# Kernel tuning notes

Measured on AMD Instinct MI355X. Metric: run time of the kernel, lower is better.

## Reference

```python
import jax, jax.numpy as jnp
import numpy as np

N, H, W, C, G, K = 8, 64, 64, 128, 8, 3
GC = C // G          # group channels = 16
P = K * K            # 9 sampling points
PAD = DIL = STRIDE = 1
OS = 1.0             # offset_scale
EPS = 1e-6
H_IN, W_IN = H + 2 * PAD, W + 2 * PAD


def _grid_sample_nhwc(img, grid):
    # img: (B, Hi, Wi, Cc) ; grid: (B, L, Pp, 2) in [-1,1]
    # bilinear, padding_mode='zeros', align_corners=False (matches F.grid_sample)
    B, Hi, Wi, Cc = img.shape
    gx = (grid[..., 0] + 1.0) * (Wi * 0.5) - 0.5
    gy = (grid[..., 1] + 1.0) * (Hi * 0.5) - 0.5
    x0 = jnp.floor(gx)
    y0 = jnp.floor(gy)
    wx1 = gx - x0
    wy1 = gy - y0
    b = jnp.arange(B).reshape(B, 1, 1)

    def tap(xi, yi, wgt):
        valid = (xi >= 0) & (xi <= Wi - 1) & (yi >= 0) & (yi <= Hi - 1)
        xc = jnp.clip(xi, 0, Wi - 1).astype(jnp.int32)
        yc = jnp.clip(yi, 0, Hi - 1).astype(jnp.int32)
        return img[b, yc, xc] * (wgt * valid)[..., None]

    return (tap(x0, y0, (1 - wx1) * (1 - wy1))
            + tap(x0 + 1, y0, wx1 * (1 - wy1))
            + tap(x0, y0 + 1, (1 - wx1) * wy1)
            + tap(x0 + 1, y0 + 1, wx1 * wy1))


def _forward(x, w_in, b_in, dw_w, dw_b, ln_g, ln_b, w_off, b_off, w_msk, b_msk, w_out, b_out):
    n = x.shape[0]
    x_proj = x @ w_in + b_in                                  # input_proj (n,H,W,C)
    # dw_conv: depthwise 3x3 -> LayerNorm(channels_last) -> GELU
    x1 = jax.lax.conv_general_dilated(
        x, dw_w, (1, 1), [((K - 1) // 2,) * 2] * 2,
        dimension_numbers=('NHWC', 'HWIO', 'NHWC'), feature_group_count=C) + dw_b
    mu = jnp.mean(x1, -1, keepdims=True)
    var = jnp.mean((x1 - mu) ** 2, -1, keepdims=True)
    x1 = (x1 - mu) * jax.lax.rsqrt(var + EPS) * ln_g + ln_b
    x1 = jax.nn.gelu(x1, approximate=False)
    offset = x1 @ w_off + b_off                               # (n,H,W,G*P*2)
    mask = jax.nn.softmax((x1 @ w_msk + b_msk).reshape(n, H, W, G, P), axis=-1)
    # reference points on the padded input (pixel-center, normalized)
    ry = (DIL * (K - 1) // 2 + 0.5 + jnp.arange(H, dtype=jnp.float32) * STRIDE) / H_IN
    rx = (DIL * (K - 1) // 2 + 0.5 + jnp.arange(W, dtype=jnp.float32) * STRIDE) / W_IN
    ref = jnp.stack([jnp.broadcast_to(rx[None, :], (H, W)),
                     jnp.broadcast_to(ry[:, None], (H, W))], -1)      # (H,W,2) = (x,y)
    # dilation kernel grid, x-major flatten (matches torch meshgrid indexing='ij')
    ks = jnp.arange(K, dtype=jnp.float32) * DIL - DIL * (K - 1) // 2
    gxk, gyk = jnp.meshgrid(ks, ks, indexing='ij')
    pts = jnp.stack([gxk / W_IN, gyk / H_IN], -1).reshape(P, 2)
    pts = jnp.tile(pts, (G, 1))                                       # (G*P,2), group-major
    loc = (ref[:, :, None, :] + pts[None, None, :, :] * OS).reshape(1, H, W, G * P * 2)
    snorm = jnp.tile(jnp.array([W_IN, H_IN], jnp.float32), G * P)     # [w,h,w,h,...]
    loc = loc + offset * OS / snorm
    grids = (2.0 * loc - 1.0).reshape(n, H * W, G, P, 2)
    grids = grids.transpose(0, 2, 1, 3, 4).reshape(n * G, H * W, P, 2)
    x_pad = jnp.pad(x_proj, ((0, 0), (PAD, PAD), (PAD, PAD), (0, 0)))
    img = x_pad.reshape(n, H_IN, W_IN, G, GC).transpose(0, 3, 1, 2, 4).reshape(n * G, H_IN, W_IN, GC)
    sampled = _grid_sample_nhwc(img, grids)                            # (n*G, HW, P, GC)
    m = mask.reshape(n, H * W, G, P).transpose(0, 2, 1, 3).reshape(n * G, H * W, P)
    out = (sampled * m[..., None]).sum(2)                              # (n*G, HW, GC)
    out = out.reshape(n, G, H * W, GC).transpose(0, 2, 1, 3).reshape(n, H, W, C)
    return out @ w_out + b_out                                         # output_proj


def setup_inputs():
    key = jax.random.key(0)
    k = jax.random.split(key, 8)
    s = 0.02
    f = jnp.float32
    return {
        'x': jax.random.normal(k[0], (N, H, W, C), f),
        'w_in': jax.random.normal(k[1], (C, C), f) * (1.0 / np.sqrt(C)),
        'b_in': jnp.zeros((C,), f),
        'dw_w': jax.random.normal(k[2], (K, K, 1, C), f) * s,
        'dw_b': jnp.zeros((C,), f),
        'ln_g': jnp.ones((C,), f),
        'ln_b': jnp.zeros((C,), f),
        'w_off': jax.random.normal(k[3], (C, G * P * 2), f) * s,
        'b_off': jax.random.normal(k[4], (G * P * 2,), f) * s,
        'w_msk': jax.random.normal(k[5], (C, G * P), f) * s,
        'b_msk': jnp.zeros((G * P,), f),
        'w_out': jax.random.normal(k[6], (C, C), f) * (1.0 / np.sqrt(C)),
        'b_out': jnp.zeros((C,), f),
    }


def reference(x, w_in, b_in, dw_w, dw_b, ln_g, ln_b, w_off, b_off, w_msk, b_msk, w_out, b_out):
    return _forward(x, w_in, b_in, dw_w, dw_b, ln_g, ln_b, w_off, b_off, w_msk, b_msk, w_out, b_out)
```

## Files before the change

kernel.cpp:

```cpp
#include <hip/hip_runtime.h>
#include <math.h>

#define NB 8
#define H 64
#define W 64
#define C 128
#define G 8
#define GC 16
#define P 9
#define NPIX (NB * H * W)
#define N_OFF 144
#define N_MSK 72
#define PXB 32
#define RECW 232
#define PK_IN_ELEMS   (8 * 4 * 64 * 8)
#define PK_COMB_ELEMS (14 * 4 * 64 * 8)
#define PK_OUT_ELEMS  (8 * 4 * 64 * 8)

using bf16x8 = __attribute__((ext_vector_type(8))) short;
using f32x4  = __attribute__((ext_vector_type(4))) float;
using u32x4  = __attribute__((ext_vector_type(4))) unsigned;

__device__ __forceinline__ short f2bf(float f) {
    union { float fv; unsigned u; } v; v.fv = f;
    unsigned r = v.u + 0x7fffu + ((v.u >> 16) & 1u);
    return (short)(r >> 16);
}

__global__ __launch_bounds__(256) void k_pack(
    const float* __restrict__ w_in, const float* __restrict__ w_off,
    const float* __restrict__ w_msk, const float* __restrict__ w_out,
    short* __restrict__ pk_in, short* __restrict__ pk_comb, short* __restrict__ pk_out)
{
    const int tid = blockIdx.x * 256 + threadIdx.x;
    int p, which;
    if (tid < PK_IN_ELEMS) { p = tid; which = 0; }
    else if (tid < PK_IN_ELEMS + PK_COMB_ELEMS) { p = tid - PK_IN_ELEMS; which = 1; }
    else if (tid < PK_IN_ELEMS + PK_COMB_ELEMS + PK_OUT_ELEMS) { p = tid - PK_IN_ELEMS - PK_COMB_ELEMS; which = 2; }
    else return;
    const int e = p & 7, lane = (p >> 3) & 63, kt = (p >> 9) & 3, nt = p >> 11;
    const int k = kt * 32 + (lane >> 4) * 8 + e;
    const int n = nt * 16 + (lane & 15);
    float v;
    if (which == 0) {
        v = w_in[k * C + n];
        pk_in[p] = f2bf(v);
    } else if (which == 1) {
        if (n < N_OFF) v = w_off[k * N_OFF + n];
        else if (n < N_OFF + N_MSK) v = w_msk[k * N_MSK + (n - N_OFF)];
        else v = 0.f;
        pk_comb[p] = f2bf(v);
    } else {
        v = w_out[k * C + n];
        pk_out[p] = f2bf(v);
    }
}

__global__ __launch_bounds__(256, 2) void k_front(
    const float* __restrict__ x, const short* __restrict__ pk_in,
    const float* __restrict__ b_in, unsigned short* __restrict__ xproj)
{
    const int t = threadIdx.x;
    const int n = blockIdx.x & 7;
    const int local = blockIdx.x >> 3;
    const int y = local >> 1;
    const int xb = (local & 1) * PXB;
    const int gpix0 = (n * H + y) * W + xb;

    const int w = t >> 6, l = t & 63;
    bf16x8 aA[2][4];
    #pragma unroll
    for (int mt = 0; mt < 2; ++mt) {
        const int m = mt * 16 + (l & 15);
        const float* rp = x + (size_t)(gpix0 + m) * C + (l >> 4) * 8;
        #pragma unroll
        for (int kt = 0; kt < 4; ++kt) {
            f32x4 v0 = *(const f32x4*)(rp + kt * 32);
            f32x4 v1 = *(const f32x4*)(rp + kt * 32 + 4);
            bf16x8 pk;
            #pragma unroll
            for (int e = 0; e < 4; ++e) { pk[e] = f2bf(v0[e]); pk[4 + e] = f2bf(v1[e]); }
            aA[mt][kt] = pk;
        }
    }
    #pragma unroll
    for (int i = 0; i < 2; ++i) {
        const int nt = w + i * 4;
        bf16x8 bf[4];
        const short* bp = pk_in + nt * 2048 + l * 8;
        #pragma unroll
        for (int kt = 0; kt < 4; ++kt) bf[kt] = *(const bf16x8*)(bp + kt * 512);
        const float bias = b_in[nt * 16 + (l & 15)];
        #pragma unroll
        for (int mt = 0; mt < 2; ++mt) {
            f32x4 acc = {0.f, 0.f, 0.f, 0.f};
            #pragma unroll
            for (int kt = 0; kt < 4; ++kt)
                acc = __builtin_amdgcn_mfma_f32_16x16x32_bf16(aA[mt][kt], bf[kt], acc, 0, 0, 0);
            const int prow = gpix0 + mt * 16 + (l >> 4) * 4;
            #pragma unroll
            for (int r = 0; r < 4; ++r)
                xproj[(size_t)(nt * NPIX + prow + r) * 16 + (l & 15)] =
                    (unsigned short)f2bf(acc[r] + bias);
        }
    }
}

__global__ __launch_bounds__(256, 2) void k_back(
    const float* __restrict__ x, const float* __restrict__ dw_w,
    const float* __restrict__ dw_b, const float* __restrict__ ln_g,
    const float* __restrict__ ln_b, const short* __restrict__ pk_comb,
    const float* __restrict__ b_off, const float* __restrict__ b_msk,
    const unsigned short* __restrict__ xproj, const short* __restrict__ pk_out,
    const float* __restrict__ b_out, float* __restrict__ out)
{
    __shared__ __align__(16) short buf0[PXB * C];
    __shared__ unsigned short recs[PXB * RECW];

    const int t = threadIdx.x;
    const int n = blockIdx.x & 7;
    const int local = blockIdx.x >> 3;
    const int y = local >> 1;
    const int xb = (local & 1) * PXB;
    const int gpix0 = (n * H + y) * W + xb;
    const int imgbase = n * (H * W);

    const int px = t >> 3;
    const int c8 = t & 7;
    const int cb = c8 * 4;
    const int sw = (px & 7) << 4;

    float a[16];
    #pragma unroll
    for (int q = 0; q < 4; ++q) {
        f32x4 v = *(const f32x4*)(dw_b + cb + q * 32);
        #pragma unroll
        for (int e = 0; e < 4; ++e) a[q * 4 + e] = v[e];
    }
    #pragma unroll
    for (int ky = 0; ky < 3; ++ky) {
        const int yy = y + ky - 1;
        if (yy < 0 || yy >= H) continue;
        #pragma unroll
        for (int kx = 0; kx < 3; ++kx) {
            const int xx = xb + px + kx - 1;
            if (xx < 0 || xx >= W) continue;
            const float* xp = x + ((size_t)(n * H + yy) * W + xx) * C;
            const float* wp = dw_w + (ky * 3 + kx) * C;
            #pragma unroll
            for (int q = 0; q < 4; ++q) {
                f32x4 xv = *(const f32x4*)(xp + cb + q * 32);
                f32x4 wv = *(const f32x4*)(wp + cb + q * 32);
                #pragma unroll
                for (int e = 0; e < 4; ++e)
                    a[q * 4 + e] = fmaf(xv[e], wv[e], a[q * 4 + e]);
            }
        }
    }
    float mu, rsg;
    {
        float s = 0.f, sq = 0.f;
        #pragma unroll
        for (int cc = 0; cc < 16; ++cc) { s += a[cc]; sq = fmaf(a[cc], a[cc], sq); }
        #pragma unroll
        for (int d = 1; d < 8; d <<= 1) {
            s += __shfl_xor(s, d);
            sq += __shfl_xor(sq, d);
        }
        mu = s * (1.0f / C);
        const float va = sq * (1.0f / C) - mu * mu;
        rsg = rsqrtf(va + 1e-6f);
    }
    #pragma unroll
    for (int q = 0; q < 4; ++q) {
        f32x4 gv = *(const f32x4*)(ln_g + cb + q * 32);
        f32x4 bv = *(const f32x4*)(ln_b + cb + q * 32);
        unsigned short h4[4];
        #pragma unroll
        for (int e = 0; e < 4; ++e) {
            float v = (a[q * 4 + e] - mu) * rsg * gv[e] + bv[e];
            h4[e] = (unsigned short)f2bf(v * 0.5f * (1.f + erff(v * 0.70710678118654752f)));
        }
        const unsigned lo = ((unsigned)h4[0]) | (((unsigned)h4[1]) << 16);
        const unsigned hi = ((unsigned)h4[2]) | (((unsigned)h4[3]) << 16);
        *(unsigned long long*)((char*)buf0 + px * 256 + ((cb * 2 + q * 64) ^ sw)) =
            ((unsigned long long)hi << 32) | lo;
    }
    __syncthreads();

    {
        const int w = t >> 6, l = t & 63;
        const int swA = (l & 7) << 4;
        bf16x8 aB[2][4];
        #pragma unroll
        for (int mt = 0; mt < 2; ++mt) {
            const int m = mt * 16 + (l & 15);
            #pragma unroll
            for (int kt = 0; kt < 4; ++kt)
                aB[mt][kt] = *(const bf16x8*)((char*)buf0 + m * 256 +
                                              ((kt * 64 + (l >> 4) * 16) ^ swA));
        }
        #pragma unroll
        for (int i = 0; i < 4; ++i) {
            const int nt = w + i * 4;
            if (nt < 14) {
                bf16x8 bf[4];
                const short* bp = pk_comb + nt * 2048 + l * 8;
                #pragma unroll
                for (int kt = 0; kt < 4; ++kt) bf[kt] = *(const bf16x8*)(bp + kt * 512);
                const int col = nt * 16 + (l & 15);
                int dcol = col;
                float bias = 0.f;
                bool valid = true;
                if (col < N_OFF) bias = b_off[col];
                else {
                    const int cm = col - N_OFF;
                    if (cm < N_MSK) {
                        const int g = (cm * 57) >> 9;
                        dcol = 144 + g * 10 + (cm - 9 * g);
                        bias = b_msk[cm];
                    } else valid = false;
                }
                #pragma unroll
                for (int mt = 0; mt < 2; ++mt) {
                    f32x4 acc = {0.f, 0.f, 0.f, 0.f};
                    #pragma unroll
                    for (int kt = 0; kt < 4; ++kt)
                        acc = __builtin_amdgcn_mfma_f32_16x16x32_bf16(aB[mt][kt], bf[kt], acc, 0, 0, 0);
                    if (valid) {
                        const int pr0 = mt * 16 + (l >> 4) * 4;
                        #pragma unroll
                        for (int r = 0; r < 4; ++r)
                            recs[(pr0 + r) * RECW + dcol] = (unsigned short)f2bf(acc[r] + bias);
                    }
                }
            }
        }
    }
    __syncthreads();

    {
        const int spx = t >> 3, g = t & 7;
        unsigned short* row = recs + spx * RECW + 144 + g * 10;
        float lg[P];
        #pragma unroll
        for (int p = 0; p < P; ++p) lg[p] = __uint_as_float(((unsigned)row[p]) << 16);
        float mx = lg[0];
        #pragma unroll
        for (int p2 = 1; p2 < P; ++p2) mx = fmaxf(mx, lg[p2]);
        float e[P], s = 0.f;
        #pragma unroll
        for (int p2 = 0; p2 < P; ++p2) { e[p2] = expf(lg[p2] - mx); s += e[p2]; }
        const float inv = 1.0f / s;
        #pragma unroll
        for (int p2 = 0; p2 < P; ++p2) row[p2] = (unsigned short)f2bf(e[p2] * inv);
    }
    __syncthreads();

    {
        const int spx = t & 31, g = t >> 5;
        const int xabs = xb + spx;
        const int swz = (spx & 7) << 4;
        const unsigned* rec32 = (const unsigned*)recs + spx * (RECW / 2);
        const unsigned short* prp = recs + spx * RECW + 144 + g * 10;

        float cf[25];
        #pragma unroll
        for (int i = 0; i < 25; ++i) cf[i] = 0.f;
        float amax = 0.f;
        #pragma unroll
        for (int p = 0; p < P; ++p) {
            const unsigned ovp = rec32[g * 9 + p];
            const float m = __uint_as_float(((unsigned)prp[p]) << 16);
            const float ox = __uint_as_float(ovp << 16);
            const float oy = __uint_as_float(ovp & 0xffff0000u);
            amax = fmaxf(amax, fmaxf(fabsf(ox), fabsf(oy)));
            const float fx = floorf(ox);
            const float fy = floorf(oy);
            const float wx = ox - fx, wy = oy - fy;
            const bool lox = fx < -0.5f;
            const bool loy = fy < -0.5f;
            const float wc0 = lox ? (1.f - wx) : 0.f;
            const float wc1 = lox ? wx : (1.f - wx);
            const float wc2 = lox ? 0.f : wx;
            const float wr0 = loy ? (1.f - wy) : 0.f;
            const float wr1 = loy ? wy : (1.f - wy);
            const float wr2 = loy ? 0.f : wy;
            const float mr0 = m * wr0, mr1 = m * wr1, mr2 = m * wr2;
            const int base = (p % 3) * 5 + (p / 3);
            cf[base + 0]  = fmaf(wc0, mr0, cf[base + 0]);
            cf[base + 1]  = fmaf(wc1, mr0, cf[base + 1]);
            cf[base + 2]  = fmaf(wc2, mr0, cf[base + 2]);
            cf[base + 5]  = fmaf(wc0, mr1, cf[base + 5]);
            cf[base + 6]  = fmaf(wc1, mr1, cf[base + 6]);
            cf[base + 7]  = fmaf(wc2, mr1, cf[base + 7]);
            cf[base + 10] = fmaf(wc0, mr2, cf[base + 10]);
            cf[base + 11] = fmaf(wc1, mr2, cf[base + 11]);
            cf[base + 12] = fmaf(wc2, mr2, cf[base + 12]);
        }
        #pragma unroll
        for (int j = 0; j < 5; ++j) {
            const int xc = xabs + j - 2;
            if (!((xc >= 0) & (xc < W))) {
                #pragma unroll
                for (int i = 0; i < 5; ++i) cf[i * 5 + j] = 0.f;
            }
        }
        #pragma unroll
        for (int i = 0; i < 5; ++i) {
            const int yc = y + i - 2;
            if (!((yc >= 0) & (yc < H))) {
                #pragma unroll
                for (int j = 0; j < 5; ++j) cf[i * 5 + j] = 0.f;
            }
        }
        const char* pb = (const char*)(xproj + (size_t)(g * NPIX + imgbase) * 16);
        int rowoff[5], coloff[5];
        #pragma unroll
        for (int i = 0; i < 5; ++i) {
            rowoff[i] = min(max(y + i - 2, 0), H - 1) * (W * 32);
            coloff[i] = min(max(xabs + i - 2, 0), W - 1) * 32;
        }

        float acc[16];
        #pragma unroll
        for (int q = 0; q < 16; ++q) acc[q] = 0.f;

        if (amax < 1.0f) {
            #pragma unroll
            for (int i = 0; i < 5; ++i) {
                #pragma unroll
                for (int j = 0; j < 5; ++j) {
                    const float c = cf[i * 5 + j];
                    const char* ap = pb + (rowoff[i] + coloff[j]);
                    u32x4 v0 = *(const u32x4*)ap;
                    u32x4 v1 = *(const u32x4*)(ap + 16);
                    #pragma unroll
                    for (int e = 0; e < 4; ++e) {
                        acc[2 * e]         = fmaf(c, __uint_as_float(v0[e] << 16), acc[2 * e]);
                        acc[2 * e + 1]     = fmaf(c, __uint_as_float(v0[e] & 0xffff0000u), acc[2 * e + 1]);
                        acc[8 + 2 * e]     = fmaf(c, __uint_as_float(v1[e] << 16), acc[8 + 2 * e]);
                        acc[8 + 2 * e + 1] = fmaf(c, __uint_as_float(v1[e] & 0xffff0000u), acc[8 + 2 * e + 1]);
                    }
                }
            }
        } else {
            for (int p = 0; p < P; ++p) {
                const unsigned ovp = rec32[g * 9 + p];
                const float m = __uint_as_float(((unsigned)prp[p]) << 16);
                const float ux = (float)(xabs + (p / 3) - 1) + __uint_as_float(ovp << 16);
                const float uy = (float)(y + (p % 3) - 1) + __uint_as_float(ovp & 0xffff0000u);
                const float fx = floorf(ux), fy = floorf(uy);
                const float wx = ux - fx, wy = uy - fy;
                const int x0 = (int)fx, y0 = (int)fy;
                float w4[4];
                w4[0] = m * (1.f - wx) * (1.f - wy);
                w4[1] = m * wx * (1.f - wy);
                w4[2] = m * (1.f - wx) * wy;
                w4[3] = m * wx * wy;
                if (!((x0 >= 0) & (x0 < W)))       { w4[0] = 0.f; w4[2] = 0.f; }
                if (!((x0 >= -1) & (x0 < W - 1)))  { w4[1] = 0.f; w4[3] = 0.f; }
                if (!((y0 >= 0) & (y0 < H)))       { w4[0] = 0.f; w4[1] = 0.f; }
                if (!((y0 >= -1) & (y0 < H - 1)))  { w4[2] = 0.f; w4[3] = 0.f; }
                const int xc[2] = { min(max(x0, 0), W - 1), min(max(x0 + 1, 0), W - 1) };
                const int yc[2] = { min(max(y0, 0), H - 1), min(max(y0 + 1, 0), H - 1) };
                for (int cn = 0; cn < 4; ++cn) {
                    const float wgt = w4[cn];
                    if (wgt == 0.f) continue;
                    const char* ap = pb + ((size_t)(yc[cn >> 1] * W + xc[cn & 1]) * 32);
                    u32x4 v0 = *(const u32x4*)ap;
                    u32x4 v1 = *(const u32x4*)(ap + 16);
                    #pragma unroll
                    for (int e = 0; e < 4; ++e) {
                        acc[2 * e]         = fmaf(wgt, __uint_as_float(v0[e] << 16), acc[2 * e]);
                        acc[2 * e + 1]     = fmaf(wgt, __uint_as_float(v0[e] & 0xffff0000u), acc[2 * e + 1]);
                        acc[8 + 2 * e]     = fmaf(wgt, __uint_as_float(v1[e] << 16), acc[8 + 2 * e]);
                        acc[8 + 2 * e + 1] = fmaf(wgt, __uint_as_float(v1[e] & 0xffff0000u), acc[8 + 2 * e + 1]);
                    }
                }
            }
        }
        __syncthreads();
        #pragma unroll
        for (int h = 0; h < 2; ++h) {
            bf16x8 pk;
            #pragma unroll
            for (int e = 0; e < 8; ++e) pk[e] = f2bf(acc[h * 8 + e]);
            *(bf16x8*)((char*)buf0 + spx * 256 + ((g * 32 + h * 16) ^ swz)) = pk;
        }
    }
    __syncthreads();

    {
        const int w = t >> 6, l = t & 63;
        const int swA = (l & 7) << 4;
        bf16x8 aS[2][4];
        #pragma unroll
        for (int mt = 0; mt < 2; ++mt) {
            const int m = mt * 16 + (l & 15);
            #pragma unroll
            for (int kt = 0; kt < 4; ++kt)
                aS[mt][kt] = *(const bf16x8*)((char*)buf0 + m * 256 +
                                              ((kt * 64 + (l >> 4) * 16) ^ swA));
        }
        #pragma unroll
        for (int i = 0; i < 2; ++i) {
            const int nt = w + i * 4;
            bf16x8 bf[4];
            const short* bp = pk_out + nt * 2048 + l * 8;
            #pragma unroll
            for (int kt = 0; kt < 4; ++kt) bf[kt] = *(const bf16x8*)(bp + kt * 512);
            const float bias = b_out[nt * 16 + (l & 15)];
            #pragma unroll
            for (int mt = 0; mt < 2; ++mt) {
                f32x4 acc2 = {0.f, 0.f, 0.f, 0.f};
                #pragma unroll
                for (int kt = 0; kt < 4; ++kt)
                    acc2 = __builtin_amdgcn_mfma_f32_16x16x32_bf16(aS[mt][kt], bf[kt], acc2, 0, 0, 0);
                const int row0 = gpix0 + mt * 16 + (l >> 4) * 4;
                #pragma unroll
                for (int r = 0; r < 4; ++r)
                    out[(size_t)(row0 + r) * C + nt * 16 + (l & 15)] = acc2[r] + bias;
            }
        }
    }
}

extern "C" void kernel_launch(void* const* d_in, const int* in_sizes, int n_in,
                              void* d_out, int out_size, void* d_ws, size_t ws_size,
                              hipStream_t stream)
{
    const float* x     = (const float*)d_in[0];
    const float* w_in  = (const float*)d_in[1];
    const float* b_in  = (const float*)d_in[2];
    const float* dw_w  = (const float*)d_in[3];
    const float* dw_b  = (const float*)d_in[4];
    const float* ln_g  = (const float*)d_in[5];
    const float* ln_b  = (const float*)d_in[6];
    const float* w_off = (const float*)d_in[7];
    const float* b_off = (const float*)d_in[8];
    const float* w_msk = (const float*)d_in[9];
    const float* b_msk = (const float*)d_in[10];
    const float* w_out = (const float*)d_in[11];
    const float* b_out = (const float*)d_in[12];

    short* pk_in   = (short*)d_ws;
    short* pk_comb = pk_in + PK_IN_ELEMS;
    short* pk_out  = pk_comb + PK_COMB_ELEMS;
    unsigned short* xproj = (unsigned short*)(pk_out + PK_OUT_ELEMS);
    float* out     = (float*)d_out;

    hipLaunchKernelGGL(k_pack, dim3(240), dim3(256), 0, stream,
                       w_in, w_off, w_msk, w_out, pk_in, pk_comb, pk_out);
    hipLaunchKernelGGL(k_front, dim3(NPIX / PXB), dim3(256), 0, stream,
                       x, pk_in, b_in, xproj);
    hipLaunchKernelGGL(k_back, dim3(NPIX / PXB), dim3(256), 0, stream,
                       x, dw_w, dw_b, ln_g, ln_b, pk_comb, b_off, b_msk,
                       xproj, pk_out, b_out, out);
}
```

Measured before the change: 52.76 us.

## Merge input projection and offset/mask branch into one launch, split sampling kernel

Restructures the kernel pipeline. The input projection and the dwconv/LN/GELU/offset-mask GEMM now run as two independent block roles inside a single launch, so they can execute concurrently. The offset/mask records are staged through the output buffer as scratch, and a separate sampling kernel reads them back, computes the softmax and does the bilinear gather plus output projection. This lets the two front stages overlap and lightens each block, at the cost of an extra global round trip for the records and softmax work repeated across lanes.

```diff
diff --git a/kernel.cpp b/kernel.cpp
--- a/kernel.cpp
+++ b/kernel.cpp
@@ -56,74 +56,66 @@
     }
 }
 
-__global__ __launch_bounds__(256, 2) void k_front(
+__global__ __launch_bounds__(256, 2) void k_main1(
     const float* __restrict__ x, const short* __restrict__ pk_in,
-    const float* __restrict__ b_in, unsigned short* __restrict__ xproj)
+    const float* __restrict__ b_in, const float* __restrict__ dw_w,
+    const float* __restrict__ dw_b, const float* __restrict__ ln_g,
+    const float* __restrict__ ln_b, const short* __restrict__ pk_comb,
+    const float* __restrict__ b_off, const float* __restrict__ b_msk,
+    unsigned short* __restrict__ xproj, float* __restrict__ out)
 {
+    __shared__ __align__(16) short x1s[PXB * C];
+    __shared__ unsigned short recs[PXB * RECW];
+
     const int t = threadIdx.x;
-    const int n = blockIdx.x & 7;
-    const int local = blockIdx.x >> 3;
+    const int role = blockIdx.x >> 10;
+    const int bid = blockIdx.x & 1023;
+    const int n = bid & 7;
+    const int local = bid >> 3;
     const int y = local >> 1;
     const int xb = (local & 1) * PXB;
     const int gpix0 = (n * H + y) * W + xb;
 
-    const int w = t >> 6, l = t & 63;
-    bf16x8 aA[2][4];
-    #pragma unroll
-    for (int mt = 0; mt < 2; ++mt) {
-        const int m = mt * 16 + (l & 15);
-        const float* rp = x + (size_t)(gpix0 + m) * C + (l >> 4) * 8;
-        #pragma unroll
-        for (int kt = 0; kt < 4; ++kt) {
-            f32x4 v0 = *(const f32x4*)(rp + kt * 32);
-            f32x4 v1 = *(const f32x4*)(rp + kt * 32 + 4);
-            bf16x8 pk;
-            #pragma unroll
-            for (int e = 0; e < 4; ++e) { pk[e] = f2bf(v0[e]); pk[4 + e] = f2bf(v1[e]); }
-            aA[mt][kt] = pk;
-        }
-    }
-    #pragma unroll
-    for (int i = 0; i < 2; ++i) {
-        const int nt = w + i * 4;
-        bf16x8 bf[4];
-        const short* bp = pk_in + nt * 2048 + l * 8;
-        #pragma unroll
-        for (int kt = 0; kt < 4; ++kt) bf[kt] = *(const bf16x8*)(bp + kt * 512);
-        const float bias = b_in[nt * 16 + (l & 15)];
+    if (role == 0) {
+        const int w = t >> 6, l = t & 63;
+        bf16x8 aA[2][4];
         #pragma unroll
         for (int mt = 0; mt < 2; ++mt) {
-            f32x4 acc = {0.f, 0.f, 0.f, 0.f};
-            #pragma unroll
-            for (int kt = 0; kt < 4; ++kt)
-                acc = __builtin_amdgcn_mfma_f32_16x16x32_bf16(aA[mt][kt], bf[kt], acc, 0, 0, 0);
-            const int prow = gpix0 + mt * 16 + (l >> 4) * 4;
-            #pragma unroll
-            for (int r = 0; r < 4; ++r)
-                xproj[(size_t)(nt * NPIX + prow + r) * 16 + (l & 15)] =
-                    (unsigned short)f2bf(acc[r] + bias);
-        }
-    }
-}
-
-__global__ __launch_bounds__(256, 2) void k_back(
-    const float* __restrict__ x, const float* __restrict__ dw_w,
-    const float* __restrict__ dw_b, const float* __restrict__ ln_g,
-    const float* __restrict__ ln_b, const short* __restrict__ pk_comb,
-    const float* __restrict__ b_off, const float* __restrict__ b_msk,
-    const unsigned short* __restrict__ xproj, const short* __restrict__ pk_out,
-    const float* __restrict__ b_out, float* __restrict__ out)
-{
-    __shared__ __align__(16) short buf0[PXB * C];
-    __shared__ unsigned short recs[PXB * RECW];
-
-    const int t = threadIdx.x;
-    const int n = blockIdx.x & 7;
-    const int local = blockIdx.x >> 3;
-    const int y = local >> 1;
-    const int xb = (local & 1) * PXB;
-    const int gpix0 = (n * H + y) * W + xb;
-    const int imgbase = n * (H * W);
+            const int m = mt * 16 + (l & 15);
+            const float* rp = x + (size_t)(gpix0 + m) * C + (l >> 4) * 8;
+            #pragma unroll
+            for (int kt = 0; kt < 4; ++kt) {
+                f32x4 v0 = *(const f32x4*)(rp + kt * 32);
+                f32x4 v1 = *(const f32x4*)(rp + kt * 32 + 4);
+                bf16x8 pk;
+                #pragma unroll
+                for (int e = 0; e < 4; ++e) { pk[e] = f2bf(v0[e]); pk[4 + e] = f2bf(v1[e]); }
+                aA[mt][kt] = pk;
+            }
+        }
+        #pragma unroll
+        for (int i = 0; i < 2; ++i) {
+            const int nt = w + i * 4;
+            bf16x8 bf[4];
+            const short* bp = pk_in + nt * 2048 + l * 8;
+            #pragma unroll
+            for (int kt = 0; kt < 4; ++kt) bf[kt] = *(const bf16x8*)(bp + kt * 512);
+            const float bias = b_in[nt * 16 + (l & 15)];
+            #pragma unroll
+            for (int mt = 0; mt < 2; ++mt) {
+                f32x4 acc = {0.f, 0.f, 0.f, 0.f};
+                #pragma unroll
+                for (int kt = 0; kt < 4; ++kt)
+                    acc = __builtin_amdgcn_mfma_f32_16x16x32_bf16(aA[mt][kt], bf[kt], acc, 0, 0, 0);
+                const int prow = gpix0 + mt * 16 + (l >> 4) * 4;
+                #pragma unroll
+                for (int r = 0; r < 4; ++r)
+                    xproj[(size_t)(nt * NPIX + prow + r) * 16 + (l & 15)] =
+                        (unsigned short)f2bf(acc[r] + bias);
+            }
+        }
+        return;
+    }
 
     const int px = t >> 3;
     const int c8 = t & 7;
@@ -183,7 +175,7 @@
         }
         const unsigned lo = ((unsigned)h4[0]) | (((unsigned)h4[1]) << 16);
         const unsigned hi = ((unsigned)h4[2]) | (((unsigned)h4[3]) << 16);
-        *(unsigned long long*)((char*)buf0 + px * 256 + ((cb * 2 + q * 64) ^ sw)) =
+        *(unsigned long long*)((char*)x1s + px * 256 + ((cb * 2 + q * 64) ^ sw)) =
             ((unsigned long long)hi << 32) | lo;
     }
     __syncthreads();
@@ -197,7 +189,7 @@
             const int m = mt * 16 + (l & 15);
             #pragma unroll
             for (int kt = 0; kt < 4; ++kt)
-                aB[mt][kt] = *(const bf16x8*)((char*)buf0 + m * 256 +
+                aB[mt][kt] = *(const bf16x8*)((char*)x1s + m * 256 +
                                               ((kt * 64 + (l >> 4) * 16) ^ swA));
         }
         #pragma unroll
@@ -240,154 +232,189 @@
     __syncthreads();
 
     {
-        const int spx = t >> 3, g = t & 7;
-        unsigned short* row = recs + spx * RECW + 144 + g * 10;
+        const int spx = t >> 3, q0 = t & 7;
+        const char* srcL = (const char*)recs + spx * (RECW * 2);
+        char* dst = (char*)out + (size_t)(gpix0 + spx) * 512;
+        #pragma unroll
+        for (int h = 0; h < 4; ++h) {
+            const int q = q0 + h * 8;
+            if (q < 28)
+                *(bf16x8*)(dst + q * 16) = *(const bf16x8*)(srcL + q * 16);
+        }
+    }
+}
+
+__global__ __launch_bounds__(256, 2) void k_samp(
+    const unsigned short* __restrict__ xproj, const short* __restrict__ pk_out,
+    const float* __restrict__ b_out, float* __restrict__ out)
+{
+    __shared__ __align__(16) short smp[PXB * C];
+
+    const int t = threadIdx.x;
+    const int n = blockIdx.x & 7;
+    const int local = blockIdx.x >> 3;
+    const int y = local >> 1;
+    const int xb = (local & 1) * PXB;
+    const int gpix0 = (n * H + y) * W + xb;
+    const int imgbase = n * (H * W);
+
+    const int spx = t & 31;
+    const int g = t >> 5;
+    const int xabs = xb + spx;
+    const int swz = (spx & 7) << 4;
+    const unsigned* slot = (const unsigned*)((const char*)out +
+                           (size_t)(gpix0 + spx) * 512);
+
+    float m9[P];
+    unsigned ov[P];
+    {
+        u32x4 a0 = *(const u32x4*)(slot + g * 9);
+        u32x4 a1 = *(const u32x4*)(slot + g * 9 + 4);
+        ov[0]=a0[0]; ov[1]=a0[1]; ov[2]=a0[2]; ov[3]=a0[3];
+        ov[4]=a1[0]; ov[5]=a1[1]; ov[6]=a1[2]; ov[7]=a1[3];
+        ov[8] = slot[g * 9 + 8];
+        u32x4 b0 = *(const u32x4*)(slot + 72 + 5 * g);
+        const unsigned pb4 = slot[72 + 5 * g + 4];
         float lg[P];
         #pragma unroll
-        for (int p = 0; p < P; ++p) lg[p] = __uint_as_float(((unsigned)row[p]) << 16);
+        for (int i = 0; i < 4; ++i) {
+            lg[2 * i] = __uint_as_float(b0[i] << 16);
+            lg[2 * i + 1] = __uint_as_float(b0[i] & 0xffff0000u);
+        }
+        lg[8] = __uint_as_float(pb4 << 16);
         float mx = lg[0];
         #pragma unroll
-        for (int p2 = 1; p2 < P; ++p2) mx = fmaxf(mx, lg[p2]);
-        float e[P], s = 0.f;
-        #pragma unroll
-        for (int p2 = 0; p2 < P; ++p2) { e[p2] = expf(lg[p2] - mx); s += e[p2]; }
+        for (int i = 1; i < P; ++i) mx = fmaxf(mx, lg[i]);
+        float s = 0.f;
+        #pragma unroll
+        for (int i = 0; i < P; ++i) { m9[i] = expf(lg[i] - mx); s += m9[i]; }
         const float inv = 1.0f / s;
         #pragma unroll
-        for (int p2 = 0; p2 < P; ++p2) row[p2] = (unsigned short)f2bf(e[p2] * inv);
-    }
-    __syncthreads();
-
-    {
-        const int spx = t & 31, g = t >> 5;
-        const int xabs = xb + spx;
-        const int swz = (spx & 7) << 4;
-        const unsigned* rec32 = (const unsigned*)recs + spx * (RECW / 2);
-        const unsigned short* prp = recs + spx * RECW + 144 + g * 10;
-
-        float cf[25];
-        #pragma unroll
-        for (int i = 0; i < 25; ++i) cf[i] = 0.f;
-        float amax = 0.f;
-        #pragma unroll
+        for (int i = 0; i < P; ++i) m9[i] *= inv;
+    }
+
+    float cf[25];
+    #pragma unroll
+    for (int i = 0; i < 25; ++i) cf[i] = 0.f;
+    float amax = 0.f;
+    #pragma unroll
+    for (int p = 0; p < P; ++p) {
+        const float m = m9[p];
+        const float ox = __uint_as_float(ov[p] << 16);
+        const float oy = __uint_as_float(ov[p] & 0xffff0000u);
+        amax = fmaxf(amax, fmaxf(fabsf(ox), fabsf(oy)));
+        const float fx = floorf(ox);
+        const float fy = floorf(oy);
+        const float wx = ox - fx, wy = oy - fy;
+        const bool lox = fx < -0.5f;
+        const bool loy = fy < -0.5f;
+        const float wc0 = lox ? (1.f - wx) : 0.f;
+        const float wc1 = lox ? wx : (1.f - wx);
+        const float wc2 = lox ? 0.f : wx;
+        const float wr0 = loy ? (1.f - wy) : 0.f;
+        const float wr1 = loy ? wy : (1.f - wy);
+        const float wr2 = loy ? 0.f : wy;
+        const float mr0 = m * wr0, mr1 = m * wr1, mr2 = m * wr2;
+        const int base = (p % 3) * 5 + (p / 3);
+        cf[base + 0]  = fmaf(wc0, mr0, cf[base + 0]);
+        cf[base + 1]  = fmaf(wc1, mr0, cf[base + 1]);
+        cf[base + 2]  = fmaf(wc2, mr0, cf[base + 2]);
+        cf[base + 5]  = fmaf(wc0, mr1, cf[base + 5]);
+        cf[base + 6]  = fmaf(wc1, mr1, cf[base + 6]);
+        cf[base + 7]  = fmaf(wc2, mr1, cf[base + 7]);
+        cf[base + 10] = fmaf(wc0, mr2, cf[base + 10]);
+        cf[base + 11] = fmaf(wc1, mr2, cf[base + 11]);
+        cf[base + 12] = fmaf(wc2, mr2, cf[base + 12]);
+    }
+    #pragma unroll
+    for (int j = 0; j < 5; ++j) {
+        const int xc = xabs + j - 2;
+        if (!((xc >= 0) & (xc < W))) {
+            #pragma unroll
+            for (int i = 0; i < 5; ++i) cf[i * 5 + j] = 0.f;
+        }
+    }
+    #pragma unroll
+    for (int i = 0; i < 5; ++i) {
+        const int yc = y + i - 2;
+        if (!((yc >= 0) & (yc < H))) {
+            #pragma unroll
+            for (int j = 0; j < 5; ++j) cf[i * 5 + j] = 0.f;
+        }
+    }
+
+    const char* pb = (const char*)(xproj + (size_t)(g * NPIX + imgbase) * 16);
+    int rowoff[5], coloff[5];
+    #pragma unroll
+    for (int i = 0; i < 5; ++i) {
+        rowoff[i] = min(max(y + i - 2, 0), H - 1) * (W * 32);
+        coloff[i] = min(max(xabs + i - 2, 0), W - 1) * 32;
+    }
+
+    float acc[16];
+    #pragma unroll
+    for (int q = 0; q < 16; ++q) acc[q] = 0.f;
+
+    if (amax < 1.0f) {
+        #pragma unroll
+        for (int i = 0; i < 5; ++i) {
+            #pragma unroll
+            for (int j = 0; j < 5; ++j) {
+                const float c = cf[i * 5 + j];
+                const char* ap = pb + (rowoff[i] + coloff[j]);
+                u32x4 v0 = *(const u32x4*)ap;
+                u32x4 v1 = *(const u32x4*)(ap + 16);
+                #pragma unroll
+                for (int e = 0; e < 4; ++e) {
+                    acc[2 * e]         = fmaf(c, __uint_as_float(v0[e] << 16), acc[2 * e]);
+                    acc[2 * e + 1]     = fmaf(c, __uint_as_float(v0[e] & 0xffff0000u), acc[2 * e + 1]);
+                    acc[8 + 2 * e]     = fmaf(c, __uint_as_float(v1[e] << 16), acc[8 + 2 * e]);
+                    acc[8 + 2 * e + 1] = fmaf(c, __uint_as_float(v1[e] & 0xffff0000u), acc[8 + 2 * e + 1]);
+                }
+            }
+        }
+    } else {
         for (int p = 0; p < P; ++p) {
-            const unsigned ovp = rec32[g * 9 + p];
-            const float m = __uint_as_float(((unsigned)prp[p]) << 16);
-            const float ox = __uint_as_float(ovp << 16);
-            const float oy = __uint_as_float(ovp & 0xffff0000u);
-            amax = fmaxf(amax, fmaxf(fabsf(ox), fabsf(oy)));
-            const float fx = floorf(ox);
-            const float fy = floorf(oy);
-            const float wx = ox - fx, wy = oy - fy;
-            const bool lox = fx < -0.5f;
-            const bool loy = fy < -0.5f;
-            const float wc0 = lox ? (1.f - wx) : 0.f;
-            const float wc1 = lox ? wx : (1.f - wx);
-            const float wc2 = lox ? 0.f : wx;
-            const float wr0 = loy ? (1.f - wy) : 0.f;
-            const float wr1 = loy ? wy : (1.f - wy);
-            const float wr2 = loy ? 0.f : wy;
-            const float mr0 = m * wr0, mr1 = m * wr1, mr2 = m * wr2;
-            const int base = (p % 3) * 5 + (p / 3);
-            cf[base + 0]  = fmaf(wc0, mr0, cf[base + 0]);
-            cf[base + 1]  = fmaf(wc1, mr0, cf[base + 1]);
-            cf[base + 2]  = fmaf(wc2, mr0, cf[base + 2]);
-            cf[base + 5]  = fmaf(wc0, mr1, cf[base + 5]);
-            cf[base + 6]  = fmaf(wc1, mr1, cf[base + 6]);
-            cf[base + 7]  = fmaf(wc2, mr1, cf[base + 7]);
-            cf[base + 10] = fmaf(wc0, mr2, cf[base + 10]);
-            cf[base + 11] = fmaf(wc1, mr2, cf[base + 11]);
-            cf[base + 12] = fmaf(wc2, mr2, cf[base + 12]);
-        }
-        #pragma unroll
-        for (int j = 0; j < 5; ++j) {
-            const int xc = xabs + j - 2;
-            if (!((xc >= 0) & (xc < W))) {
-                #pragma unroll
-                for (int i = 0; i < 5; ++i) cf[i * 5 + j] = 0.f;
-            }
-        }
-        #pragma unroll
-        for (int i = 0; i < 5; ++i) {
-            const int yc = y + i - 2;
-            if (!((yc >= 0) & (yc < H))) {
-                #pragma unroll
-                for (int j = 0; j < 5; ++j) cf[i * 5 + j] = 0.f;
-            }
-        }
-        const char* pb = (const char*)(xproj + (size_t)(g * NPIX + imgbase) * 16);
-        int rowoff[5], coloff[5];
-        #pragma unroll
-        for (int i = 0; i < 5; ++i) {
-            rowoff[i] = min(max(y + i - 2, 0), H - 1) * (W * 32);
-            coloff[i] = min(max(xabs + i - 2, 0), W - 1) * 32;
-        }
-
-        float acc[16];
-        #pragma unroll
-        for (int q = 0; q < 16; ++q) acc[q] = 0.f;
-
-        if (amax < 1.0f) {
-            #pragma unroll
-            for (int i = 0; i < 5; ++i) {
-                #pragma unroll
-                for (int j = 0; j < 5; ++j) {
-                    const float c = cf[i * 5 + j];
-                    const char* ap = pb + (rowoff[i] + coloff[j]);
-                    u32x4 v0 = *(const u32x4*)ap;
-                    u32x4 v1 = *(const u32x4*)(ap + 16);
-                    #pragma unroll
-                    for (int e = 0; e < 4; ++e) {
-                        acc[2 * e]         = fmaf(c, __uint_as_float(v0[e] << 16), acc[2 * e]);
-                        acc[2 * e + 1]     = fmaf(c, __uint_as_float(v0[e] & 0xffff0000u), acc[2 * e + 1]);
-                        acc[8 + 2 * e]     = fmaf(c, __uint_as_float(v1[e] << 16), acc[8 + 2 * e]);
-                        acc[8 + 2 * e + 1] = fmaf(c, __uint_as_float(v1[e] & 0xffff0000u), acc[8 + 2 * e + 1]);
-                    }
+            const float m = m9[p];
+            const float ux = (float)(xabs + (p / 3) - 1) + __uint_as_float(ov[p] << 16);
+            const float uy = (float)(y + (p % 3) - 1) + __uint_as_float(ov[p] & 0xffff0000u);
+            const float fx = floorf(ux), fy = floorf(uy);
+            const float wx = ux - fx, wy = uy - fy;
+            const int x0 = (int)fx, y0 = (int)fy;
+            float w4[4];
+            w4[0] = m * (1.f - wx) * (1.f - wy);
+            w4[1] = m * wx * (1.f - wy);
+            w4[2] = m * (1.f - wx) * wy;
+            w4[3] = m * wx * wy;
+            if (!((x0 >= 0) & (x0 < W)))       { w4[0] = 0.f; w4[2] = 0.f; }
+            if (!((x0 >= -1) & (x0 < W - 1)))  { w4[1] = 0.f; w4[3] = 0.f; }
+            if (!((y0 >= 0) & (y0 < H)))       { w4[0] = 0.f; w4[1] = 0.f; }
+            if (!((y0 >= -1) & (y0 < H - 1)))  { w4[2] = 0.f; w4[3] = 0.f; }
+            const int xc[2] = { min(max(x0, 0), W - 1), min(max(x0 + 1, 0), W - 1) };
+            const int yc[2] = { min(max(y0, 0), H - 1), min(max(y0 + 1, 0), H - 1) };
+            for (int cn = 0; cn < 4; ++cn) {
+                const float wgt = w4[cn];
+                if (wgt == 0.f) continue;
+                const char* ap = pb + ((size_t)(yc[cn >> 1] * W + xc[cn & 1]) * 32);
+                u32x4 v0 = *(const u32x4*)ap;
+                u32x4 v1 = *(const u32x4*)(ap + 16);
+                #pragma unroll
+                for (int e = 0; e < 4; ++e) {
+                    acc[2 * e]         = fmaf(wgt, __uint_as_float(v0[e] << 16), acc[2 * e]);
+                    acc[2 * e + 1]     = fmaf(wgt, __uint_as_float(v0[e] & 0xffff0000u), acc[2 * e + 1]);
+                    acc[8 + 2 * e]     = fmaf(wgt, __uint_as_float(v1[e] << 16), acc[8 + 2 * e]);
+                    acc[8 + 2 * e + 1] = fmaf(wgt, __uint_as_float(v1[e] & 0xffff0000u), acc[8 + 2 * e + 1]);
                 }
             }
-        } else {
-            for (int p = 0; p < P; ++p) {
-                const unsigned ovp = rec32[g * 9 + p];
-                const float m = __uint_as_float(((unsigned)prp[p]) << 16);
-                const float ux = (float)(xabs + (p / 3) - 1) + __uint_as_float(ovp << 16);
-                const float uy = (float)(y + (p % 3) - 1) + __uint_as_float(ovp & 0xffff0000u);
-                const float fx = floorf(ux), fy = floorf(uy);
-                const float wx = ux - fx, wy = uy - fy;
-                const int x0 = (int)fx, y0 = (int)fy;
-                float w4[4];
-                w4[0] = m * (1.f - wx) * (1.f - wy);
-                w4[1] = m * wx * (1.f - wy);
-                w4[2] = m * (1.f - wx) * wy;
-                w4[3] = m * wx * wy;
-                if (!((x0 >= 0) & (x0 < W)))       { w4[0] = 0.f; w4[2] = 0.f; }
-                if (!((x0 >= -1) & (x0 < W - 1)))  { w4[1] = 0.f; w4[3] = 0.f; }
-                if (!((y0 >= 0) & (y0 < H)))       { w4[0] = 0.f; w4[1] = 0.f; }
-                if (!((y0 >= -1) & (y0 < H - 1)))  { w4[2] = 0.f; w4[3] = 0.f; }
-                const int xc[2] = { min(max(x0, 0), W - 1), min(max(x0 + 1, 0), W - 1) };
-                const int yc[2] = { min(max(y0, 0), H - 1), min(max(y0 + 1, 0), H - 1) };
-                for (int cn = 0; cn < 4; ++cn) {
-                    const float wgt = w4[cn];
-                    if (wgt == 0.f) continue;
-                    const char* ap = pb + ((size_t)(yc[cn >> 1] * W + xc[cn & 1]) * 32);
-                    u32x4 v0 = *(const u32x4*)ap;
-                    u32x4 v1 = *(const u32x4*)(ap + 16);
-                    #pragma unroll
-                    for (int e = 0; e < 4; ++e) {
-                        acc[2 * e]         = fmaf(wgt, __uint_as_float(v0[e] << 16), acc[2 * e]);
-                        acc[2 * e + 1]     = fmaf(wgt, __uint_as_float(v0[e] & 0xffff0000u), acc[2 * e + 1]);
-                        acc[8 + 2 * e]     = fmaf(wgt, __uint_as_float(v1[e] << 16), acc[8 + 2 * e]);
-                        acc[8 + 2 * e + 1] = fmaf(wgt, __uint_as_float(v1[e] & 0xffff0000u), acc[8 + 2 * e + 1]);
-                    }
-                }
-            }
-        }
-        __syncthreads();
-        #pragma unroll
-        for (int h = 0; h < 2; ++h) {
-            bf16x8 pk;
-            #pragma unroll
-            for (int e = 0; e < 8; ++e) pk[e] = f2bf(acc[h * 8 + e]);
-            *(bf16x8*)((char*)buf0 + spx * 256 + ((g * 32 + h * 16) ^ swz)) = pk;
-        }
+        }
+    }
+
+    #pragma unroll
+    for (int h = 0; h < 2; ++h) {
+        bf16x8 pk;
+        #pragma unroll
+        for (int e = 0; e < 8; ++e) pk[e] = f2bf(acc[h * 8 + e]);
+        *(bf16x8*)((char*)smp + spx * 256 + ((g * 32 + h * 16) ^ swz)) = pk;
     }
     __syncthreads();
 
@@ -400,7 +427,7 @@
             const int m = mt * 16 + (l & 15);
             #pragma unroll
             for (int kt = 0; kt < 4; ++kt)
-                aS[mt][kt] = *(const bf16x8*)((char*)buf0 + m * 256 +
+                aS[mt][kt] = *(const bf16x8*)((char*)smp + m * 256 +
                                               ((kt * 64 + (l >> 4) * 16) ^ swA));
         }
         #pragma unroll
@@ -452,9 +479,9 @@
 
     hipLaunchKernelGGL(k_pack, dim3(240), dim3(256), 0, stream,
                        w_in, w_off, w_msk, w_out, pk_in, pk_comb, pk_out);
-    hipLaunchKernelGGL(k_front, dim3(NPIX / PXB), dim3(256), 0, stream,
-                       x, pk_in, b_in, xproj);
-    hipLaunchKernelGGL(k_back, dim3(NPIX / PXB), dim3(256), 0, stream,
-                       x, dw_w, dw_b, ln_g, ln_b, pk_comb, b_off, b_msk,
+    hipLaunchKernelGGL(k_main1, dim3(2 * (NPIX / PXB)), dim3(256), 0, stream,
+                       x, pk_in, b_in, dw_w, dw_b, ln_g, ln_b,
+                       pk_comb, b_off, b_msk, xproj, out);
+    hipLaunchKernelGGL(k_samp, dim3(NPIX / PXB), dim3(256), 0, stream,
                        xproj, pk_out, b_out, out);
 }
```

Result: no change. 53.68 us (+1.7%).
